# Kernel optimization log

Measured on AMD Instinct MI355X. Metric: run time of the kernel, lower is better.

The kernel has to match this reference:

```python
import jax, jax.numpy as jnp
import numpy as np

MASK_VALUE = -10000.0


def setup_inputs() -> dict:
    key = jax.random.key(0)
    ks = jax.random.split(key, 6)
    F_, H, L1N, L2N, B = 1024, 2048, 64, 256, 8192

    def w(k, shape, fan_in):
        return jax.random.normal(k, shape, jnp.float32) * (1.0 / np.sqrt(fan_in))

    x = jax.random.normal(ks[0], (B, F_), jnp.float32)
    W1_1 = w(ks[1], (F_, H), F_); b1_1 = jnp.zeros((H,), jnp.float32)
    W1_2 = w(ks[2], (H, L1N), H); b1_2 = jnp.zeros((L1N,), jnp.float32)
    W2_1 = w(ks[3], (F_, H), F_); b2_1 = jnp.zeros((H,), jnp.float32)
    W2_2 = w(ks[4], (2 * H, L2N), 2 * H); b2_2 = jnp.zeros((L2N,), jnp.float32)
    # child_parent[j] = L1 parent of L2 label j (contiguous groups of 4),
    # equivalent to L12_table = [[4i,4i+1,4i+2,4i+3] for i in range(64)]
    child_parent = jnp.arange(L2N, dtype=jnp.int32) // (L2N // L1N)
    return dict(x=x, W1_1=W1_1, b1_1=b1_1, W1_2=W1_2, b1_2=b1_2,
                W2_1=W2_1, b2_1=b2_1, W2_2=W2_2, b2_2=b2_2,
                child_parent=child_parent)


def reference(x, W1_1, b1_1, W1_2, b1_2, W2_1, b2_1, W2_2, b2_2, child_parent):
    h1 = jax.nn.relu(x @ W1_1 + b1_1)          # [B, H]
    h2 = jax.nn.relu(x @ W2_1 + b2_1)          # [B, H]
    cat = jnp.concatenate([h1, h2], axis=1)    # [B, 2H]
    L1 = jax.nn.softmax(jax.nn.relu(h1 @ W1_2 + b1_2), axis=1)   # [B, L1N]
    l2_logits = jax.nn.relu(cat @ W2_2 + b2_2)                   # [B, L2N]
    parent = jnp.argmax(L1, axis=1)                              # [B] int
    # mask[i, j] = 0 if L2 label j is a child of argmax L1 label, else MASK_VALUE
    mask = jnp.where(child_parent[None, :] == parent[:, None], 0.0, MASK_VALUE)
    L2 = jax.nn.softmax(l2_logits + mask, axis=1)
    return (L1, L2)
```

## Files before the change

kernel.cpp:

```cpp
#include <hip/hip_runtime.h>
#include <hip/hip_bf16.h>
#include <stdint.h>
#include <math.h>


typedef _Float16 f16x8 __attribute__((ext_vector_type(8)));
typedef float    f32x4 __attribute__((ext_vector_type(4)));

#define MASK_VALUE (-10000.0f)
#define SWZ(r) ((((r) + ((r) >> 2))) & 3)
#define RSCALE 2048.0f
#define INV_RSCALE (1.0f / 2048.0f)

#define GLOBAL_AS __attribute__((address_space(1)))
#define LDS_AS    __attribute__((address_space(3)))

__device__ __forceinline__ void gload16(const void* g, void* lds) {
    __builtin_amdgcn_global_load_lds((const GLOBAL_AS void*)g, (LDS_AS void*)lds, 16, 0, 0);
}

__device__ __forceinline__ float rd_any(const void* p, size_t i, int flag) {
    return flag ? (float)((const __hip_bfloat16*)p)[i] : ((const float*)p)[i];
}

__global__ void detect_dtype(const unsigned int* __restrict__ x, int* __restrict__ flag) {
    __shared__ int cnt;
    if (threadIdx.x == 0) cnt = 0;
    __syncthreads();
    int local = 0;
#pragma unroll
    for (int i = 0; i < 4; ++i) {
        unsigned int w = x[threadIdx.x * 4 + i];
        unsigned int e = (w >> 7) & 0xFFu;
        if (e >= 96u && e <= 144u) local++;
    }
    atomicAdd(&cnt, local);
    __syncthreads();
    if (threadIdx.x == 0) *flag = (cnt >= 600) ? 1 : 0;
}

__global__ void prep_all(
    const void* __restrict__ x, const void* __restrict__ W1_1,
    const void* __restrict__ W2_1, const void* __restrict__ W2_2,
    const void* __restrict__ W1_2,
    _Float16* __restrict__ xh, _Float16* __restrict__ xl,
    _Float16* __restrict__ whT, _Float16* __restrict__ wlT,
    _Float16* __restrict__ W2Tf, _Float16* __restrict__ W22Tf,
    _Float16* __restrict__ w12h, _Float16* __restrict__ w12l,
    const int* __restrict__ flagp)
{
    __shared__ __align__(16) float tile[64][65];
    int flag = *flagp;
    int bid = blockIdx.x, t = threadIdx.x;
    int tx = t & 63, ty = t >> 6;

    if (bid < 8192) {
        size_t i = ((size_t)bid * 256 + t) * 4;
#pragma unroll
        for (int j = 0; j < 4; ++j) {
            float a = rd_any(x, i + j, flag);
            _Float16 h = (_Float16)a;
            xh[i + j] = h;
            xl[i + j] = (_Float16)((a - (float)h) * RSCALE);
        }
        return;
    }

    if (bid < 8704) {
        int b = bid - 8192;
        int c0 = (b & 31) * 64, r0 = (b >> 5) * 64;
#pragma unroll
        for (int i = 0; i < 16; ++i) {
            int r = ty + i * 4;
            tile[r][tx] = rd_any(W1_1, (size_t)(r0 + r) * 2048 + c0 + tx, flag);
        }
        __syncthreads();
#pragma unroll
        for (int i = 0; i < 16; ++i) {
            int r = ty + i * 4;
            size_t o = (size_t)(c0 + r) * 1024 + r0 + tx;
            float a = tile[tx][r];
            _Float16 h = (_Float16)a;
            whT[o] = h;
            wlT[o] = (_Float16)((a - (float)h) * RSCALE);
        }
        return;
    }

    if (bid < 9216) {
        int b = bid - 8704;
        int c0 = (b & 31) * 64, r0 = (b >> 5) * 64;
#pragma unroll
        for (int i = 0; i < 16; ++i) {
            int r = ty + i * 4;
            tile[r][tx] = rd_any(W2_1, (size_t)(r0 + r) * 2048 + c0 + tx, flag);
        }
        __syncthreads();
#pragma unroll
        for (int i = 0; i < 16; ++i) {
            int r = ty + i * 4;
            W2Tf[(size_t)(c0 + r) * 1024 + r0 + tx] = (_Float16)tile[tx][r];
        }
        return;
    }

    if (bid < 9472) {
        int b = bid - 9216;
        int c0 = (b & 3) * 64, r0 = (b >> 2) * 64;
#pragma unroll
        for (int i = 0; i < 16; ++i) {
            int r = ty + i * 4;
            tile[r][tx] = rd_any(W2_2, (size_t)(r0 + r) * 256 + c0 + tx, flag);
        }
        __syncthreads();
#pragma unroll
        for (int i = 0; i < 16; ++i) {
            int r = ty + i * 4;
            W22Tf[(size_t)(c0 + r) * 4096 + r0 + tx] = (_Float16)tile[tx][r];
        }
        return;
    }

    {
        int b = bid - 9472;
        int r0 = b * 64;
#pragma unroll
        for (int i = 0; i < 16; ++i) {
            int r = ty + i * 4;
            tile[r][tx] = rd_any(W1_2, (size_t)(r0 + r) * 64 + tx, flag);
        }
        __syncthreads();
#pragma unroll
        for (int i = 0; i < 16; ++i) {
            int r = ty + i * 4;
            size_t o = (size_t)r * 2048 + r0 + tx;
            float a = tile[tx][r];
            _Float16 h = (_Float16)a;
            w12h[o] = h;
            w12l[o] = (_Float16)((a - (float)h) * RSCALE);
        }
    }
}

__global__ __launch_bounds__(256, 2) void h12_gemm(
    const _Float16* __restrict__ xh, const _Float16* __restrict__ xl,
    const _Float16* __restrict__ whT, const _Float16* __restrict__ wlT,
    const void* __restrict__ b11,
    const _Float16* __restrict__ W2Tf, const void* __restrict__ b21,
    _Float16* __restrict__ h1h, _Float16* __restrict__ h1l,
    _Float16* __restrict__ h2b,
    const int* __restrict__ flagp)
{
    constexpr int K = 1024, BK = 32;
    __shared__ __align__(16) char smem[36864];
    int flag = *flagp;
    int t = threadIdx.x, w = t >> 6, lane = t & 63;
    int wr = w & 1, wcb = w >> 1;
    int ml = lane & 15, q = lane >> 4;
    int rq = (lane >> 4) * 4;

    if (blockIdx.x < 1024) {
        _Float16* Ah = (_Float16*)smem;
        _Float16* Al = (_Float16*)(smem + 8192);
        _Float16* Bh = (_Float16*)(smem + 16384);
        _Float16* Bl = (_Float16*)(smem + 24576);
        int bid = blockIdx.x;
        int g = bid & 7, s = bid >> 3;
        int mt = g * 8 + (s & 7), nt = s >> 3;
        int i0 = mt * 128, j0 = nt * 128;

        f32x4 acc1[4][4], acc2[4][4];
#pragma unroll
        for (int a = 0; a < 4; ++a)
#pragma unroll
            for (int b = 0; b < 4; ++b) {
                acc1[a][b] = (f32x4){0.f, 0.f, 0.f, 0.f};
                acc2[a][b] = (f32x4){0.f, 0.f, 0.f, 0.f};
            }

        for (int kt = 0; kt < K; kt += BK) {
            __syncthreads();
#pragma unroll
            for (int qq = 0; qq < 2; ++qq) {
                int c = qq * 256 + t;
                int row = c >> 2;
                int gc = (c & 3) ^ SWZ(row);
                size_t ga = (size_t)(i0 + row) * K + kt + gc * 8;
                size_t gb = (size_t)(j0 + row) * K + kt + gc * 8;
                gload16(xh + ga, (char*)Ah + c * 16);
                gload16(xl + ga, (char*)Al + c * 16);
                gload16(whT + gb, (char*)Bh + c * 16);
                gload16(wlT + gb, (char*)Bl + c * 16);
            }
            __syncthreads();

            f16x8 bh[4], bl[4];
#pragma unroll
            for (int ct = 0; ct < 4; ++ct) {
                int row = wcb * 64 + ct * 16 + ml;
                int off = row * 32 + ((q ^ SWZ(row)) << 3);
                bh[ct] = *(const f16x8*)(Bh + off);
                bl[ct] = *(const f16x8*)(Bl + off);
            }
#pragma unroll
            for (int rt = 0; rt < 4; ++rt) {
                int row = wr * 64 + rt * 16 + ml;
                int off = row * 32 + ((q ^ SWZ(row)) << 3);
                f16x8 ah = *(const f16x8*)(Ah + off);
                f16x8 al = *(const f16x8*)(Al + off);
#pragma unroll
                for (int ct = 0; ct < 4; ++ct) {
                    acc1[rt][ct] = __builtin_amdgcn_mfma_f32_16x16x32_f16(ah, bh[ct], acc1[rt][ct], 0, 0, 0);
                    acc2[rt][ct] = __builtin_amdgcn_mfma_f32_16x16x32_f16(ah, bl[ct], acc2[rt][ct], 0, 0, 0);
                    acc2[rt][ct] = __builtin_amdgcn_mfma_f32_16x16x32_f16(al, bh[ct], acc2[rt][ct], 0, 0, 0);
                }
            }
        }

#pragma unroll
        for (int ct = 0; ct < 4; ++ct) {
            float bv = rd_any(b11, j0 + wcb * 64 + ct * 16 + ml, flag);
#pragma unroll
            for (int rt = 0; rt < 4; ++rt)
#pragma unroll
                for (int r = 0; r < 4; ++r) {
                    float v = acc1[rt][ct][r] + acc2[rt][ct][r] * INV_RSCALE + bv;
                    acc1[rt][ct][r] = v > 0.f ? v : 0.f;
                }
        }

        _Float16* C = (_Float16*)smem;
#pragma unroll
        for (int p = 0; p < 2; ++p) {
            __syncthreads();
#pragma unroll
            for (int rt = 0; rt < 4; ++rt)
#pragma unroll
                for (int ct = 0; ct < 4; ++ct)
#pragma unroll
                    for (int r = 0; r < 4; ++r) {
                        float v = acc1[rt][ct][r];
                        _Float16 h = (_Float16)v;
                        _Float16 outv = (p == 0) ? h
                                      : (_Float16)((v - (float)h) * RSCALE);
                        int rl = wr * 64 + rt * 16 + rq + r;
                        int cl = wcb * 64 + ct * 16 + ml;
                        C[rl * 136 + cl] = outv;
                    }
            __syncthreads();
            _Float16* dst = (p == 0) ? h1h : h1l;
#pragma unroll
            for (int i = 0; i < 8; ++i) {
                int c = i * 256 + t;
                int row = c >> 4, c8 = (c & 15) * 8;
                *(f16x8*)(dst + (size_t)(i0 + row) * 2048 + j0 + c8) =
                    *(const f16x8*)(C + row * 136 + c8);
            }
        }
    } else {
        _Float16* As = (_Float16*)smem;
        _Float16* Bs = (_Float16*)(smem + 8192);
        int bid = blockIdx.x - 1024;
        int g = bid & 7, s = bid >> 3;
        int mt = g * 8 + (s & 7), nt = s >> 3;
        int i0 = mt * 128, j0 = nt * 128;

        f32x4 acc[4][4];
#pragma unroll
        for (int a = 0; a < 4; ++a)
#pragma unroll
            for (int b = 0; b < 4; ++b) acc[a][b] = (f32x4){0.f, 0.f, 0.f, 0.f};

        for (int kt = 0; kt < K; kt += BK) {
            __syncthreads();
#pragma unroll
            for (int qq = 0; qq < 2; ++qq) {
                int c = qq * 256 + t;
                int row = c >> 2;
                int gc = (c & 3) ^ SWZ(row);
                gload16(xh + (size_t)(i0 + row) * K + kt + gc * 8, (char*)As + c * 16);
                gload16(W2Tf + (size_t)(j0 + row) * K + kt + gc * 8, (char*)Bs + c * 16);
            }
            __syncthreads();
            f16x8 af[4], bf[4];
#pragma unroll
            for (int rt = 0; rt < 4; ++rt) {
                int row = wr * 64 + rt * 16 + ml;
                af[rt] = *(const f16x8*)(As + row * 32 + ((q ^ SWZ(row)) << 3));
            }
#pragma unroll
            for (int ct = 0; ct < 4; ++ct) {
                int row = wcb * 64 + ct * 16 + ml;
                bf[ct] = *(const f16x8*)(Bs + row * 32 + ((q ^ SWZ(row)) << 3));
            }
#pragma unroll
            for (int rt = 0; rt < 4; ++rt)
#pragma unroll
                for (int ct = 0; ct < 4; ++ct)
                    acc[rt][ct] = __builtin_amdgcn_mfma_f32_16x16x32_f16(
                        af[rt], bf[ct], acc[rt][ct], 0, 0, 0);
        }

        _Float16* C = (_Float16*)smem;
        __syncthreads();
#pragma unroll
        for (int ct = 0; ct < 4; ++ct) {
            float bv = rd_any(b21, j0 + wcb * 64 + ct * 16 + ml, flag);
#pragma unroll
            for (int rt = 0; rt < 4; ++rt)
#pragma unroll
                for (int r = 0; r < 4; ++r) {
                    float v = acc[rt][ct][r] + bv;
                    v = v > 0.f ? v : 0.f;
                    int rl = wr * 64 + rt * 16 + rq + r;
                    int cl = wcb * 64 + ct * 16 + ml;
                    C[rl * 136 + cl] = (_Float16)v;
                }
        }
        __syncthreads();
#pragma unroll
        for (int i = 0; i < 8; ++i) {
            int c = i * 256 + t;
            int row = c >> 4, c8 = (c & 15) * 8;
            *(f16x8*)(h2b + (size_t)(i0 + row) * 2048 + j0 + c8) =
                *(const f16x8*)(C + row * 136 + c8);
        }
    }
}

__global__ __launch_bounds__(256, 2) void head_fused(
    const _Float16* __restrict__ h1h, const _Float16* __restrict__ h1l,
    const _Float16* __restrict__ h2b, const _Float16* __restrict__ W22T,
    float* __restrict__ partials,
    const _Float16* __restrict__ w12h, const _Float16* __restrict__ w12l,
    const void* __restrict__ b12, float* __restrict__ L1out,
    int* __restrict__ parent, const int* __restrict__ flagp)
{
    constexpr int BK = 32;
    __shared__ __align__(16) char smem[16384];
    int flag = *flagp;
    int t = threadIdx.x, w = t >> 6, lane = t & 63;
    int ml = lane & 15, q = lane >> 4;

    if (blockIdx.x < 512) {
        _Float16* As = (_Float16*)smem;
        _Float16* Bs = (_Float16*)(smem + 8192);
        int bid = blockIdx.x;
        int g = bid & 7, s = bid >> 3;
        int mt = g * 8 + (s & 7);
        int rest = s >> 3;
        int nt = rest & 1, kc = rest >> 1;
        int i0 = mt * 128, j0 = nt * 128;
        const _Float16* Abase = (kc < 2) ? h1h : h2b;
        int kof = (kc & 1) * 1024;
        int wr = w & 1, wcb = w >> 1;

        f32x4 acc[4][4];
#pragma unroll
        for (int a = 0; a < 4; ++a)
#pragma unroll
            for (int b = 0; b < 4; ++b) acc[a][b] = (f32x4){0.f, 0.f, 0.f, 0.f};

        for (int kt = 0; kt < 1024; kt += BK) {
            __syncthreads();
#pragma unroll
            for (int qq = 0; qq < 2; ++qq) {
                int c = qq * 256 + t;
                int row = c >> 2;
                int gc = (c & 3) ^ SWZ(row);
                gload16(Abase + (size_t)(i0 + row) * 2048 + kof + kt + gc * 8, (char*)As + c * 16);
                gload16(W22T + (size_t)(j0 + row) * 4096 + kc * 1024 + kt + gc * 8, (char*)Bs + c * 16);
            }
            __syncthreads();
            f16x8 af[4], bf[4];
#pragma unroll
            for (int rt = 0; rt < 4; ++rt) {
                int row = wr * 64 + rt * 16 + ml;
                af[rt] = *(const f16x8*)(As + row * 32 + ((q ^ SWZ(row)) << 3));
            }
#pragma unroll
            for (int ct = 0; ct < 4; ++ct) {
                int row = wcb * 64 + ct * 16 + ml;
                bf[ct] = *(const f16x8*)(Bs + row * 32 + ((q ^ SWZ(row)) << 3));
            }
#pragma unroll
            for (int rt = 0; rt < 4; ++rt)
#pragma unroll
                for (int ct = 0; ct < 4; ++ct)
                    acc[rt][ct] = __builtin_amdgcn_mfma_f32_16x16x32_f16(
                        af[rt], bf[ct], acc[rt][ct], 0, 0, 0);
        }

        float* out = partials + (size_t)kc * 8192 * 256;
        int rq = (lane >> 4) * 4;
#pragma unroll
        for (int ct = 0; ct < 4; ++ct) {
            int nl = j0 + wcb * 64 + ct * 16 + ml;
#pragma unroll
            for (int rt = 0; rt < 4; ++rt) {
                int mbase = i0 + wr * 64 + rt * 16 + rq;
#pragma unroll
                for (int r = 0; r < 4; ++r)
                    out[(size_t)(mbase + r) * 256 + nl] = acc[rt][ct][r];
            }
        }
    } else {
        float* red = (float*)smem;
        int r0 = (blockIdx.x - 512) * 16;
        int kq = (lane >> 4) * 8;

        f32x4 acch[4], accx[4];
#pragma unroll
        for (int ct = 0; ct < 4; ++ct) {
            acch[ct] = (f32x4){0.f, 0.f, 0.f, 0.f};
            accx[ct] = (f32x4){0.f, 0.f, 0.f, 0.f};
        }

        size_t aoff = (size_t)(r0 + ml) * 2048 + w * 512 + kq;
        const _Float16* Ah = h1h + aoff;
        const _Float16* Al = h1l + aoff;
        size_t boff[4];
#pragma unroll
        for (int ct = 0; ct < 4; ++ct)
            boff[ct] = (size_t)(ct * 16 + ml) * 2048 + w * 512 + kq;

        f16x8 ah = *(const f16x8*)(Ah), al = *(const f16x8*)(Al);
        f16x8 bh[4], bl[4];
#pragma unroll
        for (int ct = 0; ct < 4; ++ct) {
            bh[ct] = *(const f16x8*)(w12h + boff[ct]);
            bl[ct] = *(const f16x8*)(w12l + boff[ct]);
        }

        for (int kt = 0; kt < 512; kt += 32) {
            int nk = (kt + 32) & 511;
            f16x8 nah = *(const f16x8*)(Ah + nk);
            f16x8 nal = *(const f16x8*)(Al + nk);
            f16x8 nbh[4], nbl[4];
#pragma unroll
            for (int ct = 0; ct < 4; ++ct) {
                nbh[ct] = *(const f16x8*)(w12h + boff[ct] + nk);
                nbl[ct] = *(const f16x8*)(w12l + boff[ct] + nk);
            }
#pragma unroll
            for (int ct = 0; ct < 4; ++ct) {
                acch[ct] = __builtin_amdgcn_mfma_f32_16x16x32_f16(ah, bh[ct], acch[ct], 0, 0, 0);
                accx[ct] = __builtin_amdgcn_mfma_f32_16x16x32_f16(ah, bl[ct], accx[ct], 0, 0, 0);
                accx[ct] = __builtin_amdgcn_mfma_f32_16x16x32_f16(al, bh[ct], accx[ct], 0, 0, 0);
            }
            ah = nah; al = nal;
#pragma unroll
            for (int ct = 0; ct < 4; ++ct) { bh[ct] = nbh[ct]; bl[ct] = nbl[ct]; }
        }

        f32x4 acc[4];
#pragma unroll
        for (int ct = 0; ct < 4; ++ct)
#pragma unroll
            for (int i = 0; i < 4; ++i)
                acc[ct][i] = acch[ct][i] + accx[ct][i] * INV_RSCALE;

        if (w > 0) {
#pragma unroll
            for (int ct = 0; ct < 4; ++ct)
#pragma unroll
                for (int i = 0; i < 4; ++i)
                    red[((w - 1) * 4 + ct) * 256 + lane * 4 + i] = acc[ct][i];
        }
        __syncthreads();
        if (w != 0) return;

#pragma unroll
        for (int wv = 0; wv < 3; ++wv)
#pragma unroll
            for (int ct = 0; ct < 4; ++ct)
#pragma unroll
                for (int i = 0; i < 4; ++i)
                    acc[ct][i] += red[(wv * 4 + ct) * 256 + lane * 4 + i];

        int rq = (lane >> 4) * 4;
        float vals[4][4];
        float vmax[4] = {-1e30f, -1e30f, -1e30f, -1e30f};
        int vidx[4] = {1 << 30, 1 << 30, 1 << 30, 1 << 30};
#pragma unroll
        for (int ct = 0; ct < 4; ++ct) {
            int col = ct * 16 + ml;
            float bv = rd_any(b12, col, flag);
#pragma unroll
            for (int r = 0; r < 4; ++r) {
                float v = acc[ct][r] + bv;
                v = v > 0.f ? v : 0.f;
                vals[ct][r] = v;
                if (v > vmax[r] || (v == vmax[r] && col < vidx[r])) { vmax[r] = v; vidx[r] = col; }
            }
        }
#pragma unroll
        for (int d = 1; d < 16; d <<= 1) {
#pragma unroll
            for (int r = 0; r < 4; ++r) {
                float om = __shfl_xor(vmax[r], d);
                int oi = __shfl_xor(vidx[r], d);
                if (om > vmax[r] || (om == vmax[r] && oi < vidx[r])) { vmax[r] = om; vidx[r] = oi; }
            }
        }
        float vsum[4] = {0.f, 0.f, 0.f, 0.f};
#pragma unroll
        for (int ct = 0; ct < 4; ++ct)
#pragma unroll
            for (int r = 0; r < 4; ++r) {
                float e = __expf(vals[ct][r] - vmax[r]);
                vals[ct][r] = e;
                vsum[r] += e;
            }
#pragma unroll
        for (int d = 1; d < 16; d <<= 1)
#pragma unroll
            for (int r = 0; r < 4; ++r) vsum[r] += __shfl_xor(vsum[r], d);

#pragma unroll
        for (int r = 0; r < 4; ++r) {
            float inv = 1.0f / vsum[r];
            int grow = r0 + rq + r;
#pragma unroll
            for (int ct = 0; ct < 4; ++ct)
                L1out[(size_t)grow * 64 + ct * 16 + ml] = vals[ct][r] * inv;
            if (ml == 0) parent[grow] = vidx[r];
        }
    }
}

__global__ __launch_bounds__(256, 2) void l2_softmax(
    const float* __restrict__ partials, const void* __restrict__ b22,
    const int* __restrict__ child_parent, const int* __restrict__ parent,
    float* __restrict__ L2out, const int* __restrict__ flagp)
{
    int flag = *flagp;
    int t = threadIdx.x, w = t >> 6, lane = t & 63;
    int row = blockIdx.x * 4 + w;
    int c4 = lane * 4;

    float v[4] = {0.f, 0.f, 0.f, 0.f};
#pragma unroll
    for (int kc = 0; kc < 4; ++kc) {
        float4 pv = *(const float4*)(partials + ((size_t)kc * 8192 + row) * 256 + c4);
        v[0] += pv.x; v[1] += pv.y; v[2] += pv.z; v[3] += pv.w;
    }
    int par = parent[row];
#pragma unroll
    for (int j = 0; j < 4; ++j) {
        float x = v[j] + rd_any(b22, c4 + j, flag);
        x = x > 0.f ? x : 0.f;
        if (child_parent[c4 + j] != par) x += MASK_VALUE;
        v[j] = x;
    }
    float m = fmaxf(fmaxf(v[0], v[1]), fmaxf(v[2], v[3]));
#pragma unroll
    for (int d = 1; d < 64; d <<= 1) m = fmaxf(m, __shfl_xor(m, d));
    float sum = 0.f;
#pragma unroll
    for (int j = 0; j < 4; ++j) { v[j] = __expf(v[j] - m); sum += v[j]; }
#pragma unroll
    for (int d = 1; d < 64; d <<= 1) sum += __shfl_xor(sum, d);
    float inv = 1.0f / sum;
    float4 o = {v[0] * inv, v[1] * inv, v[2] * inv, v[3] * inv};
    *(float4*)(L2out + (size_t)row * 256 + c4) = o;
}

extern "C" void kernel_launch(void* const* d_in, const int* in_sizes, int n_in,
                              void* d_out, int out_size, void* d_ws, size_t ws_size,
                              hipStream_t stream) {
    (void)in_sizes; (void)n_in; (void)out_size; (void)ws_size;

    const void* x    = d_in[0];
    const void* W1_1 = d_in[1];
    const void* b1_1 = d_in[2];
    const void* W1_2 = d_in[3];
    const void* b1_2 = d_in[4];
    const void* W2_1 = d_in[5];
    const void* b2_1 = d_in[6];
    const void* W2_2 = d_in[7];
    const void* b2_2 = d_in[8];
    const int* child_parent = (const int*)d_in[9];

    char* p = (char*)d_ws;
    _Float16* xh    = (_Float16*)(p);
    _Float16* xl    = (_Float16*)(p + 16777216);
    _Float16* whT   = (_Float16*)(p + 33554432);
    _Float16* wlT   = (_Float16*)(p + 37748736);
    _Float16* h1h   = (_Float16*)(p + 41943040);
    _Float16* h1l   = (_Float16*)(p + 75497472);
    _Float16* h2b   = (_Float16*)(p + 109051904);
    _Float16* W2Tf  = (_Float16*)(p + 142606336);
    _Float16* W22Tf = (_Float16*)(p + 146800640);
    _Float16* w12h  = (_Float16*)(p + 148897792);
    _Float16* w12l  = (_Float16*)(p + 149159936);
    float* partials = (float*)(p + 149422080);
    int* parent     = (int*)(p + 182976512);
    int* flag       = (int*)(p + 183009280);

    float* L1out = (float*)d_out;
    float* L2out = L1out + (size_t)8192 * 64;

    hipLaunchKernelGGL(detect_dtype, dim3(1), dim3(256), 0, stream,
                       (const unsigned int*)x, flag);
    hipLaunchKernelGGL(prep_all, dim3(9504), dim3(256), 0, stream,
                       x, W1_1, W2_1, W2_2, W1_2,
                       xh, xl, whT, wlT, W2Tf, W22Tf, w12h, w12l, flag);
    hipLaunchKernelGGL(h12_gemm, dim3(2048), dim3(256), 0, stream,
                       xh, xl, whT, wlT, b1_1, W2Tf, b2_1,
                       h1h, h1l, h2b, flag);
    hipLaunchKernelGGL(head_fused, dim3(1024), dim3(256), 0, stream,
                       h1h, h1l, h2b, W22Tf, partials,
                       w12h, w12l, b1_2, L1out, parent, flag);
    hipLaunchKernelGGL(l2_softmax, dim3(2048), dim3(256), 0, stream,
                       partials, b2_2, child_parent, parent, L2out, flag);
}
```

Before: 347.2 us.

## Rewrite h1/h2 GEMM as 512-thread multi-buffered pipelined kernel with larger tiles

Replaces the 256-thread, single-buffered h12 GEMM with a 512-thread kernel. The h1 path uses 256x128 tiles and the h2 path uses 256x256 tiles. Global-to-LDS loads are prefetched two k-steps ahead through a 3- or 4-stage LDS ring, with explicit vmcnt/lgkmcnt waits, split MFMA phases and s_setprio. Blocks are mapped to tiles in an XCD-aware way. The goal is to hide memory latency behind MFMA work and to raise operand reuse per block. In exchange it uses about 144KB of LDS, which limits occupancy to one block per CU, and it depends on hand-tuned wait counts being correct.

```diff
diff --git a/kernel.cpp b/kernel.cpp
--- a/kernel.cpp
+++ b/kernel.cpp
@@ -9,6 +9,7 @@
 
 #define MASK_VALUE (-10000.0f)
 #define SWZ(r) ((((r) + ((r) >> 2))) & 3)
+#define SW4(row, c) ((c) ^ (((row) >> 1) & 3))
 #define RSCALE 2048.0f
 #define INV_RSCALE (1.0f / 2048.0f)
 
@@ -22,6 +23,16 @@
 __device__ __forceinline__ float rd_any(const void* p, size_t i, int flag) {
     return flag ? (float)((const __hip_bfloat16*)p)[i] : ((const float*)p)[i];
 }
+
+__device__ __forceinline__ void wg_bar() {
+    asm volatile("" ::: "memory");
+    __builtin_amdgcn_s_barrier();
+    asm volatile("" ::: "memory");
+}
+#define LGKM0() do { asm volatile("s_waitcnt lgkmcnt(0)" ::: "memory"); \
+                     __builtin_amdgcn_sched_barrier(0); } while (0)
+#define VMW(n)  asm volatile("s_waitcnt vmcnt(" #n ")" ::: "memory")
+#define MFMA16(a,b,c) __builtin_amdgcn_mfma_f32_16x16x32_f16((a),(b),(c),0,0,0)
 
 __global__ void detect_dtype(const unsigned int* __restrict__ x, int* __restrict__ flag) {
     __shared__ int cnt;
@@ -142,7 +153,7 @@
     }
 }
 
-__global__ __launch_bounds__(256, 2) void h12_gemm(
+__global__ __launch_bounds__(512, 2) void h12_gemm8(
     const _Float16* __restrict__ xh, const _Float16* __restrict__ xl,
     const _Float16* __restrict__ whT, const _Float16* __restrict__ wlT,
     const void* __restrict__ b11,
@@ -151,23 +162,18 @@
     _Float16* __restrict__ h2b,
     const int* __restrict__ flagp)
 {
-    constexpr int K = 1024, BK = 32;
-    __shared__ __align__(16) char smem[36864];
+    __shared__ __align__(16) char smem[147456];
     int flag = *flagp;
     int t = threadIdx.x, w = t >> 6, lane = t & 63;
-    int wr = w & 1, wcb = w >> 1;
-    int ml = lane & 15, q = lane >> 4;
-    int rq = (lane >> 4) * 4;
-
-    if (blockIdx.x < 1024) {
-        _Float16* Ah = (_Float16*)smem;
-        _Float16* Al = (_Float16*)(smem + 8192);
-        _Float16* Bh = (_Float16*)(smem + 16384);
-        _Float16* Bl = (_Float16*)(smem + 24576);
-        int bid = blockIdx.x;
-        int g = bid & 7, s = bid >> 3;
-        int mt = g * 8 + (s & 7), nt = s >> 3;
-        int i0 = mt * 128, j0 = nt * 128;
+    int ml = lane & 15, q = lane >> 4, rq = q * 4;
+
+    int xcd = blockIdx.x & 7, rblk = blockIdx.x >> 3;
+
+    if (rblk < 64) {
+        int lb = xcd * 64 + rblk;
+        int mt = lb >> 4, nt = lb & 15;
+        int i0 = mt * 256, j0 = nt * 128;
+        int wr = w & 3, wc = w >> 2;
 
         f32x4 acc1[4][4], acc2[4][4];
 #pragma unroll
@@ -178,57 +184,105 @@
                 acc2[a][b] = (f32x4){0.f, 0.f, 0.f, 0.f};
             }
 
-        for (int kt = 0; kt < K; kt += BK) {
-            __syncthreads();
-#pragma unroll
-            for (int qq = 0; qq < 2; ++qq) {
-                int c = qq * 256 + t;
-                int row = c >> 2;
-                int gc = (c & 3) ^ SWZ(row);
-                size_t ga = (size_t)(i0 + row) * K + kt + gc * 8;
-                size_t gb = (size_t)(j0 + row) * K + kt + gc * 8;
-                gload16(xh + ga, (char*)Ah + c * 16);
-                gload16(xl + ga, (char*)Al + c * 16);
-                gload16(whT + gb, (char*)Bh + c * 16);
-                gload16(wlT + gb, (char*)Bl + c * 16);
-            }
-            __syncthreads();
-
-            f16x8 bh[4], bl[4];
-#pragma unroll
-            for (int ct = 0; ct < 4; ++ct) {
-                int row = wcb * 64 + ct * 16 + ml;
-                int off = row * 32 + ((q ^ SWZ(row)) << 3);
-                bh[ct] = *(const f16x8*)(Bh + off);
-                bl[ct] = *(const f16x8*)(Bl + off);
-            }
+        auto stage = [&](char* bp, int kt, int g) {
+            if (g < 4) {
+                int ci = ((g & 1) << 9) + t;
+                int row = ci >> 2;
+                int c = SW4(row, ci & 3);
+                const _Float16* src = (g < 2) ? xh : xl;
+                gload16(src + (size_t)(i0 + row) * 1024 + kt + c * 8,
+                        bp + ((g < 2) ? 0 : 16384) + ci * 16);
+            } else {
+                int ci = t;
+                int row = ci >> 2;
+                int c = SW4(row, ci & 3);
+                const _Float16* src = (g == 4) ? whT : wlT;
+                gload16(src + (size_t)(j0 + row) * 1024 + kt + c * 8,
+                        bp + ((g == 4) ? 32768 : 40960) + ci * 16);
+            }
+        };
+
+#pragma unroll
+        for (int g = 0; g < 6; ++g) stage(smem, 0, g);
+#pragma unroll
+        for (int g = 0; g < 6; ++g) stage(smem + 49152, 32, g);
+        VMW(6);
+        wg_bar();
+
+        int cur = 0;
+        for (int s = 0; s < 32; ++s) {
+            char* bp = smem + cur * 49152;
+            int cur2 = cur + 2; if (cur2 >= 3) cur2 -= 3;
+            char* bp2 = smem + cur2 * 49152;
+            int kt2 = (s + 2) * 32;
+            bool st = (s < 30);
+
+            f16x8 ah[4], al[4], bh[2], bl[2];
 #pragma unroll
             for (int rt = 0; rt < 4; ++rt) {
                 int row = wr * 64 + rt * 16 + ml;
-                int off = row * 32 + ((q ^ SWZ(row)) << 3);
-                f16x8 ah = *(const f16x8*)(Ah + off);
-                f16x8 al = *(const f16x8*)(Al + off);
-#pragma unroll
-                for (int ct = 0; ct < 4; ++ct) {
-                    acc1[rt][ct] = __builtin_amdgcn_mfma_f32_16x16x32_f16(ah, bh[ct], acc1[rt][ct], 0, 0, 0);
-                    acc2[rt][ct] = __builtin_amdgcn_mfma_f32_16x16x32_f16(ah, bl[ct], acc2[rt][ct], 0, 0, 0);
-                    acc2[rt][ct] = __builtin_amdgcn_mfma_f32_16x16x32_f16(al, bh[ct], acc2[rt][ct], 0, 0, 0);
+                int off = row * 64 + (SW4(row, q) << 4);
+                ah[rt] = *(const f16x8*)(bp + off);
+                al[rt] = *(const f16x8*)(bp + 16384 + off);
+            }
+#pragma unroll
+            for (int ct = 0; ct < 2; ++ct) {
+                int row = wc * 64 + ct * 16 + ml;
+                int off = row * 64 + (SW4(row, q) << 4);
+                bh[ct] = *(const f16x8*)(bp + 32768 + off);
+                bl[ct] = *(const f16x8*)(bp + 40960 + off);
+            }
+            if (st) { stage(bp2, kt2, 0); stage(bp2, kt2, 1); stage(bp2, kt2, 2); }
+            wg_bar();
+            LGKM0();
+            __builtin_amdgcn_s_setprio(1);
+#pragma unroll
+            for (int rt = 0; rt < 4; ++rt)
+#pragma unroll
+                for (int ct = 0; ct < 2; ++ct) {
+                    acc1[rt][ct] = MFMA16(ah[rt], bh[ct], acc1[rt][ct]);
+                    acc2[rt][ct] = MFMA16(ah[rt], bl[ct], acc2[rt][ct]);
+                    acc2[rt][ct] = MFMA16(al[rt], bh[ct], acc2[rt][ct]);
                 }
-            }
+            __builtin_amdgcn_s_setprio(0);
+            wg_bar();
+
+#pragma unroll
+            for (int ct = 0; ct < 2; ++ct) {
+                int row = wc * 64 + (ct + 2) * 16 + ml;
+                int off = row * 64 + (SW4(row, q) << 4);
+                bh[ct] = *(const f16x8*)(bp + 32768 + off);
+                bl[ct] = *(const f16x8*)(bp + 40960 + off);
+            }
+            if (st) { stage(bp2, kt2, 3); stage(bp2, kt2, 4); stage(bp2, kt2, 5); }
+            wg_bar();
+            LGKM0();
+            __builtin_amdgcn_s_setprio(1);
+#pragma unroll
+            for (int rt = 0; rt < 4; ++rt)
+#pragma unroll
+                for (int ct = 0; ct < 2; ++ct) {
+                    acc1[rt][ct + 2] = MFMA16(ah[rt], bh[ct], acc1[rt][ct + 2]);
+                    acc2[rt][ct + 2] = MFMA16(ah[rt], bl[ct], acc2[rt][ct + 2]);
+                    acc2[rt][ct + 2] = MFMA16(al[rt], bh[ct], acc2[rt][ct + 2]);
+                }
+            __builtin_amdgcn_s_setprio(0);
+            if (st) { VMW(6); } else { VMW(0); }
+            wg_bar();
+            cur = cur + 1; if (cur == 3) cur = 0;
         }
 
 #pragma unroll
         for (int ct = 0; ct < 4; ++ct) {
-            float bv = rd_any(b11, j0 + wcb * 64 + ct * 16 + ml, flag);
+            float bv = rd_any(b11, j0 + wc * 64 + ct * 16 + ml, flag);
 #pragma unroll
             for (int rt = 0; rt < 4; ++rt)
 #pragma unroll
-                for (int r = 0; r < 4; ++r) {
-                    float v = acc1[rt][ct][r] + acc2[rt][ct][r] * INV_RSCALE + bv;
-                    acc1[rt][ct][r] = v > 0.f ? v : 0.f;
+                for (int rr = 0; rr < 4; ++rr) {
+                    float v = acc1[rt][ct][rr] + acc2[rt][ct][rr] * INV_RSCALE + bv;
+                    acc1[rt][ct][rr] = v > 0.f ? v : 0.f;
                 }
         }
-
         _Float16* C = (_Float16*)smem;
 #pragma unroll
         for (int p = 0; p < 2; ++p) {
@@ -238,92 +292,132 @@
 #pragma unroll
                 for (int ct = 0; ct < 4; ++ct)
 #pragma unroll
-                    for (int r = 0; r < 4; ++r) {
-                        float v = acc1[rt][ct][r];
+                    for (int rr = 0; rr < 4; ++rr) {
+                        float v = acc1[rt][ct][rr];
                         _Float16 h = (_Float16)v;
                         _Float16 outv = (p == 0) ? h
                                       : (_Float16)((v - (float)h) * RSCALE);
-                        int rl = wr * 64 + rt * 16 + rq + r;
-                        int cl = wcb * 64 + ct * 16 + ml;
+                        int rl = wr * 64 + rt * 16 + rq + rr;
+                        int cl = wc * 64 + ct * 16 + ml;
                         C[rl * 136 + cl] = outv;
                     }
             __syncthreads();
             _Float16* dst = (p == 0) ? h1h : h1l;
 #pragma unroll
             for (int i = 0; i < 8; ++i) {
-                int c = i * 256 + t;
+                int c = i * 512 + t;
                 int row = c >> 4, c8 = (c & 15) * 8;
                 *(f16x8*)(dst + (size_t)(i0 + row) * 2048 + j0 + c8) =
                     *(const f16x8*)(C + row * 136 + c8);
             }
         }
     } else {
-        _Float16* As = (_Float16*)smem;
-        _Float16* Bs = (_Float16*)(smem + 8192);
-        int bid = blockIdx.x - 1024;
-        int g = bid & 7, s = bid >> 3;
-        int mt = g * 8 + (s & 7), nt = s >> 3;
-        int i0 = mt * 128, j0 = nt * 128;
-
-        f32x4 acc[4][4];
-#pragma unroll
-        for (int a = 0; a < 4; ++a)
+        int lb = xcd * 32 + (rblk - 64);
+        int mt = lb >> 3, nt = lb & 7;
+        int i0 = mt * 256, j0 = nt * 256;
+        int wr = w & 1, wc = w >> 1;
+
+        f32x4 acc[8][4];
+#pragma unroll
+        for (int a = 0; a < 8; ++a)
 #pragma unroll
             for (int b = 0; b < 4; ++b) acc[a][b] = (f32x4){0.f, 0.f, 0.f, 0.f};
 
-        for (int kt = 0; kt < K; kt += BK) {
-            __syncthreads();
-#pragma unroll
-            for (int qq = 0; qq < 2; ++qq) {
-                int c = qq * 256 + t;
-                int row = c >> 2;
-                int gc = (c & 3) ^ SWZ(row);
-                gload16(xh + (size_t)(i0 + row) * K + kt + gc * 8, (char*)As + c * 16);
-                gload16(W2Tf + (size_t)(j0 + row) * K + kt + gc * 8, (char*)Bs + c * 16);
-            }
-            __syncthreads();
+        auto stage = [&](char* bp, int kt, int g) {
+            int ci = ((g & 1) << 9) + t;
+            int row = ci >> 2;
+            int c = SW4(row, ci & 3);
+            if (g < 2)
+                gload16(xh + (size_t)(i0 + row) * 1024 + kt + c * 8,
+                        bp + ci * 16);
+            else
+                gload16(W2Tf + (size_t)(j0 + row) * 1024 + kt + c * 8,
+                        bp + 16384 + ci * 16);
+        };
+
+#pragma unroll
+        for (int g = 0; g < 4; ++g) stage(smem, 0, g);
+#pragma unroll
+        for (int g = 0; g < 4; ++g) stage(smem + 32768, 32, g);
+        VMW(4);
+        wg_bar();
+
+        int cur = 0;
+        for (int s = 0; s < 32; ++s) {
+            char* bp = smem + cur * 32768;
+            char* bp2 = smem + ((cur + 2) & 3) * 32768;
+            int kt2 = (s + 2) * 32;
+            bool st = (s < 30);
+
             f16x8 af[4], bf[4];
 #pragma unroll
             for (int rt = 0; rt < 4; ++rt) {
-                int row = wr * 64 + rt * 16 + ml;
-                af[rt] = *(const f16x8*)(As + row * 32 + ((q ^ SWZ(row)) << 3));
+                int row = wr * 128 + rt * 16 + ml;
+                int off = row * 64 + (SW4(row, q) << 4);
+                af[rt] = *(const f16x8*)(bp + off);
             }
 #pragma unroll
             for (int ct = 0; ct < 4; ++ct) {
-                int row = wcb * 64 + ct * 16 + ml;
-                bf[ct] = *(const f16x8*)(Bs + row * 32 + ((q ^ SWZ(row)) << 3));
-            }
+                int row = wc * 64 + ct * 16 + ml;
+                int off = row * 64 + (SW4(row, q) << 4);
+                bf[ct] = *(const f16x8*)(bp + 16384 + off);
+            }
+            if (st) { stage(bp2, kt2, 0); stage(bp2, kt2, 2); }
+            wg_bar();
+            LGKM0();
+            __builtin_amdgcn_s_setprio(1);
 #pragma unroll
             for (int rt = 0; rt < 4; ++rt)
 #pragma unroll
                 for (int ct = 0; ct < 4; ++ct)
-                    acc[rt][ct] = __builtin_amdgcn_mfma_f32_16x16x32_f16(
-                        af[rt], bf[ct], acc[rt][ct], 0, 0, 0);
+                    acc[rt][ct] = MFMA16(af[rt], bf[ct], acc[rt][ct]);
+            __builtin_amdgcn_s_setprio(0);
+            wg_bar();
+
+#pragma unroll
+            for (int rt = 0; rt < 4; ++rt) {
+                int row = wr * 128 + (rt + 4) * 16 + ml;
+                int off = row * 64 + (SW4(row, q) << 4);
+                af[rt] = *(const f16x8*)(bp + off);
+            }
+            if (st) { stage(bp2, kt2, 1); stage(bp2, kt2, 3); }
+            wg_bar();
+            LGKM0();
+            __builtin_amdgcn_s_setprio(1);
+#pragma unroll
+            for (int rt = 0; rt < 4; ++rt)
+#pragma unroll
+                for (int ct = 0; ct < 4; ++ct)
+                    acc[rt + 4][ct] = MFMA16(af[rt], bf[ct], acc[rt + 4][ct]);
+            __builtin_amdgcn_s_setprio(0);
+            if (st) { VMW(4); } else { VMW(0); }
+            wg_bar();
+            cur = (cur + 1) & 3;
         }
 
         _Float16* C = (_Float16*)smem;
         __syncthreads();
 #pragma unroll
         for (int ct = 0; ct < 4; ++ct) {
-            float bv = rd_any(b21, j0 + wcb * 64 + ct * 16 + ml, flag);
-#pragma unroll
-            for (int rt = 0; rt < 4; ++rt)
-#pragma unroll
-                for (int r = 0; r < 4; ++r) {
-                    float v = acc[rt][ct][r] + bv;
+            float bv = rd_any(b21, j0 + wc * 64 + ct * 16 + ml, flag);
+#pragma unroll
+            for (int rt = 0; rt < 8; ++rt)
+#pragma unroll
+                for (int rr = 0; rr < 4; ++rr) {
+                    float v = acc[rt][ct][rr] + bv;
                     v = v > 0.f ? v : 0.f;
-                    int rl = wr * 64 + rt * 16 + rq + r;
-                    int cl = wcb * 64 + ct * 16 + ml;
-                    C[rl * 136 + cl] = (_Float16)v;
+                    int rl = wr * 128 + rt * 16 + rq + rr;
+                    int cl = wc * 64 + ct * 16 + ml;
+                    C[rl * 264 + cl] = (_Float16)v;
                 }
         }
         __syncthreads();
 #pragma unroll
-        for (int i = 0; i < 8; ++i) {
-            int c = i * 256 + t;
-            int row = c >> 4, c8 = (c & 15) * 8;
+        for (int i = 0; i < 16; ++i) {
+            int c = i * 512 + t;
+            int row = c >> 5, c8 = (c & 31) * 8;
             *(f16x8*)(h2b + (size_t)(i0 + row) * 2048 + j0 + c8) =
-                *(const f16x8*)(C + row * 136 + c8);
+                *(const f16x8*)(C + row * 264 + c8);
         }
     }
 }
@@ -606,7 +700,7 @@
     hipLaunchKernelGGL(prep_all, dim3(9504), dim3(256), 0, stream,
                        x, W1_1, W2_1, W2_2, W1_2,
                        xh, xl, whT, wlT, W2Tf, W22Tf, w12h, w12l, flag);
-    hipLaunchKernelGGL(h12_gemm, dim3(2048), dim3(256), 0, stream,
+    hipLaunchKernelGGL(h12_gemm8, dim3(768), dim3(512), 0, stream,
                        xh, xl, whT, wlT, b1_1, W2Tf, b2_1,
                        h1h, h1l, h2b, flag);
     hipLaunchKernelGGL(head_fused, dim3(1024), dim3(256), 0, stream,
```

Result: faster. 336.8 us (-3.0%).
